# Kernel tuning notes

Measured on AMD Instinct MI355X. Metric: run time of the kernel, lower is better.

The kernel has to match this reference:

```python
import jax, jax.numpy as jnp
import numpy as np

N_QUBITS = 4
N_LAYERS = 2
KERNEL = 2
OUT_DEPTH = 4
SEED = 42          # pennylane RandomLayers default seed
RATIO_IMPRIM = 0.3 # pennylane RandomLayers default CNOT ratio


def _build_random_layers():
    """Replicates pennylane.templates.RandomLayers gate-structure sampling
    (seed=42): per layer, draw rotations from {RX,RY,RZ} on random wires
    (consuming one weight each) interleaved with CNOTs on random wire pairs."""
    rng = np.random.RandomState(SEED)
    rot_names = ['RX', 'RY', 'RZ']
    ops = []  # (name, wires, layer, weight_idx)
    for l in range(N_LAYERS):
        i = 0
        while i < 4:  # weights.shape[1] == 4
            if rng.random_sample() > RATIO_IMPRIM:
                gate = rot_names[rng.randint(3)]
                wire = int(rng.randint(N_QUBITS))
                ops.append((gate, (wire,), l, i))
                i += 1
            else:
                w = rng.choice(N_QUBITS, size=2, replace=False)
                ops.append(('CNOT', (int(w[0]), int(w[1])), l, -1))
    return tuple(ops)

OPS = _build_random_layers()

_CNOT = np.array([[1, 0, 0, 0], [0, 1, 0, 0], [0, 0, 0, 1], [0, 0, 1, 0]], dtype=np.complex64)


def _apply_1q(state, U, wire):
    # state: [P, 2,2,2,2]; U: [P,2,2] (batched) or [2,2] (shared)
    st = jnp.moveaxis(state, 1 + wire, -1)
    if U.ndim == 3:
        st = jnp.einsum('pab,p...b->p...a', U, st)
    else:
        st = jnp.einsum('ab,p...b->p...a', U, st)
    return jnp.moveaxis(st, -1, 1 + wire)


def _apply_cnot(state, c, t):
    st = jnp.moveaxis(state, (1 + c, 1 + t), (-2, -1))
    shp = st.shape
    st = st.reshape(shp[:-2] + (4,))
    st = jnp.einsum('ab,p...b->p...a', jnp.asarray(_CNOT), st)
    return jnp.moveaxis(st.reshape(shp), (-2, -1), (1 + c, 1 + t))


def _ry_batched(theta):
    # theta [P] -> [P,2,2]  (RY is real)
    c = jnp.cos(theta / 2)
    s = jnp.sin(theta / 2)
    return jnp.stack([jnp.stack([c, -s], -1), jnp.stack([s, c], -1)], -2).astype(jnp.complex64)


def _rot(name, theta):
    th = theta.astype(jnp.float32)
    c = jnp.cos(th / 2).astype(jnp.complex64)
    s = jnp.sin(th / 2).astype(jnp.complex64)
    zero = c * 0
    if name == 'RX':
        return jnp.stack([jnp.stack([c, -1j * s]), jnp.stack([-1j * s, c])])
    if name == 'RY':
        return jnp.stack([jnp.stack([c, -s]), jnp.stack([s, c])])
    # RZ
    e_m = jnp.exp(-0.5j * th.astype(jnp.complex64))
    e_p = jnp.exp(0.5j * th.astype(jnp.complex64))
    return jnp.stack([jnp.stack([e_m, zero]), jnp.stack([zero, e_p])])


def _patches(x):
    # x [1,C,H,W] -> [C*out*out, s*s], row-major pixel order matching
    # flatten(x[0, c, idx:idx+s, idy:idy+s])
    out = x.shape[3] - KERNEL + 1
    cols = [x[0, :, i:i + out, j:j + out] for i in range(KERNEL) for j in range(KERNEL)]
    p = jnp.stack(cols, axis=-1)  # [C, out, out, s*s]
    return p.reshape(-1, KERNEL * KERNEL)


def _simulate(angles, weights):
    # angles [P, n_qubits] -> PauliZ expectations [P, n_qubits]
    P = angles.shape[0]
    state = jnp.zeros((P,) + (2,) * N_QUBITS, jnp.complex64)
    state = state.at[(slice(None),) + (0,) * N_QUBITS].set(1.0)
    for j in range(N_QUBITS):  # angle encoding: RY(pi * input_j)
        state = _apply_1q(state, _ry_batched(angles[:, j]), j)
    for (name, wires, l, wi) in OPS:  # RandomLayers(weights)
        if name == 'CNOT':
            state = _apply_cnot(state, wires[0], wires[1])
        else:
            state = _apply_1q(state, _rot(name, weights[l, wi]), wires[0])
    probs = state.real ** 2 + state.imag ** 2  # [P,2,2,2,2]
    z = jnp.array([1.0, -1.0], probs.dtype)
    exps = []
    for j in range(N_QUBITS):
        other = tuple(a for a in range(1, 1 + N_QUBITS) if a != 1 + j)
        exps.append(probs.sum(axis=other) @ z)  # [P]
    return jnp.stack(exps, -1)  # [P, n_qubits]


def setup_inputs() -> dict:
    key = jax.random.key(0)
    kx, kw = jax.random.split(key)
    x = jax.random.uniform(kx, (1, 3, 512, 512), jnp.float32)
    weights = jax.random.uniform(kw, (N_LAYERS, 4), jnp.float32, 0.0, float(2 * np.pi))
    return {"x": x, "weights": weights}


def reference(x, weights):
    out_hw = x.shape[3] - KERNEL + 1
    C = x.shape[1]
    angles = jnp.pi * _patches(x)              # [C*out*out, 4]
    exps = _simulate(angles, weights)          # [C*out*out, 4]
    q_out = exps.reshape(C, out_hw, out_hw, KERNEL * KERNEL).sum(0)  # channel sum, as the idz loop
    # exact torch.reshape semantics: row-major reinterpretation of (out,out,4)
    return q_out.reshape(1, OUT_DEPTH, out_hw, out_hw)
```

## Files before the change

### kernel.cpp

```cpp
#include <hip/hip_runtime.h>
#include <stdint.h>

#define OUTHW 511
#define IMGW 512

struct COps { int n; int kind[64]; int wa[64]; int wb[64]; int widx[64]; };

struct CMT {
    uint32_t mt[624]; int mti;
    constexpr CMT(uint32_t s) : mt{}, mti(624) {
        mt[0] = s;
        for (int i = 1; i < 624; ++i)
            mt[i] = 1812433253u * (mt[i - 1] ^ (mt[i - 1] >> 30)) + (uint32_t)i;
    }
    constexpr uint32_t next32() {
        if (mti >= 624) {
            for (int i = 0; i < 624; ++i) {
                uint32_t y = (mt[i] & 0x80000000u) | (mt[(i + 1) % 624] & 0x7fffffffu);
                mt[i] = mt[(i + 397) % 624] ^ (y >> 1) ^ ((y & 1u) ? 0x9908b0dfu : 0u);
            }
            mti = 0;
        }
        uint32_t y = mt[mti++];
        y ^= y >> 11; y ^= (y << 7) & 0x9d2c5680u; y ^= (y << 15) & 0xefc60000u; y ^= y >> 18;
        return y;
    }
    constexpr double rand_double() {
        uint32_t a = next32() >> 5, b = next32() >> 6;
        return (a * 67108864.0 + b) / 9007199254740992.0;
    }
    constexpr uint32_t interval(uint32_t mx) {
        if (mx == 0) return 0;
        uint32_t mask = mx;
        mask |= mask >> 1; mask |= mask >> 2; mask |= mask >> 4;
        mask |= mask >> 8; mask |= mask >> 16;
        uint32_t v = next32() & mask;
        while (v > mx) v = next32() & mask;
        return v;
    }
};

constexpr COps build_ops_ce() {
    CMT mt(42u); COps P{}; P.n = 0;
    for (int l = 0; l < 2; ++l) {
        int i = 0;
        while (i < 4 && P.n < 64) {
            if (mt.rand_double() > 0.3) {
                int g = (int)mt.interval(2);
                int w = (int)mt.interval(3);
                P.kind[P.n] = g; P.wa[P.n] = w; P.wb[P.n] = 0; P.widx[P.n] = l * 4 + i;
                ++P.n; ++i;
            } else {
                int arr[4] = {0, 1, 2, 3};
                for (int ii = 3; ii >= 1; --ii) {
                    int j = (int)mt.interval((uint32_t)ii);
                    int t = arr[ii]; arr[ii] = arr[j]; arr[j] = t;
                }
                P.kind[P.n] = 3; P.wa[P.n] = arr[0]; P.wb[P.n] = arr[1]; P.widx[P.n] = -1;
                ++P.n;
            }
        }
    }
    return P;
}
constexpr COps OPS = build_ops_ce();

struct Tabs {
    bool u[81];
    bool mj[4][81];
    int nu;
    int tlist[81];
    int zm[81], xm[81];
};

constexpr Tabs build_tabs() {
    Tabs T{};
    for (int j = 0; j < 4; ++j) {
        bool cur[256] = {};
        cur[1 << (4 + j)] = true;
        for (int o = OPS.n - 1; o >= 0; --o) {
            bool nxt[256] = {};
            for (int c = 0; c < 256; ++c) if (cur[c]) {
                if (OPS.kind[o] == 3) {
                    int cc = OPS.wa[o], tt = OPS.wb[o], nc = c;
                    if (c & (1 << cc))       nc ^= (1 << tt);
                    if (c & (1 << (4 + tt))) nc ^= (1 << (4 + cc));
                    nxt[nc] = true;
                } else {
                    int w = OPS.wa[o];
                    int xw = (c >> w) & 1, zw = (c >> (4 + w)) & 1;
                    bool anti = false; int pm = 0;
                    if (OPS.kind[o] == 0)      { anti = zw != 0;        pm = 1 << w; }
                    else if (OPS.kind[o] == 1) { anti = (xw ^ zw) != 0; pm = (1 << w) | (1 << (4 + w)); }
                    else                       { anti = xw != 0;        pm = 1 << (4 + w); }
                    nxt[c] = true;
                    if (anti) nxt[c ^ pm] = true;
                }
            }
            for (int c = 0; c < 256; ++c) cur[c] = nxt[c];
        }
        for (int c = 0; c < 256; ++c) if (cur[c]) {
            bool hasY = false; int t = 0;
            for (int k = 0; k < 4; ++k) {
                int xk = (c >> k) & 1, zk = (c >> (4 + k)) & 1;
                if (xk && zk) hasY = true;
                t = t * 3 + (zk ? 1 : (xk ? 2 : 0));
            }
            if (!hasY) { T.mj[j][t] = true; T.u[t] = true; }
        }
    }
    T.nu = 0;
    for (int t = 0; t < 81; ++t) {
        int dd[4] = {t / 27, (t / 9) % 3, (t / 3) % 3, t % 3};
        int zm = 0, xm = 0;
        for (int k = 0; k < 4; ++k) {
            int p = 3 - k;
            if (dd[k] == 1) zm |= 1 << p;
            else if (dd[k] == 2) xm |= 1 << p;
        }
        T.zm[t] = zm; T.xm[t] = xm;
        if (T.u[t]) T.tlist[T.nu++] = t;
    }
    return T;
}
constexpr Tabs TB = build_tabs();
constexpr int NU = TB.nu;

__device__ float g_W[4 * 81];

__global__ void __launch_bounds__(512) build_table(const float* __restrict__ wts) {
    __shared__ float Ur[256];
    __shared__ float Ui[256];
    __shared__ float S[81 * 16];
    const int tid = threadIdx.x;
    if (tid < 256) {
        Ur[tid] = ((tid >> 4) == (tid & 15)) ? 1.f : 0.f;
        Ui[tid] = 0.f;
    }
    __syncthreads();
    const float INV4PI = 0.07957747154594767f;
#pragma unroll
    for (int o = 0; o < OPS.n; ++o) {
        if (OPS.kind[o] == 3) {
            const int pc = 3 - OPS.wa[o], pt = 3 - OPS.wb[o];
            if (tid < 64) {
                int b = tid >> 2, q = tid & 3;
                int rem[2]; int ri = 0;
#pragma unroll
                for (int p = 0; p < 4; ++p) if (p != pc && p != pt) rem[ri++] = p;
                int n  = (1 << pc) | ((q & 1) ? (1 << rem[0]) : 0)
                                   | (((q >> 1) & 1) ? (1 << rem[1]) : 0);
                int n2 = n | (1 << pt);
                float tr = Ur[b * 16 + n]; Ur[b * 16 + n] = Ur[b * 16 + n2]; Ur[b * 16 + n2] = tr;
                float ti = Ui[b * 16 + n]; Ui[b * 16 + n] = Ui[b * 16 + n2]; Ui[b * 16 + n2] = ti;
            }
        } else {
            const float th = wts[OPS.widx[o]];
            const float ch = __builtin_amdgcn_cosf(th * INV4PI);
            const float sh = __builtin_amdgcn_sinf(th * INV4PI);
            const int p = 3 - OPS.wa[o];
            if (tid < 128) {
                int b = tid >> 3, q = tid & 7;
                int low = q & ((1 << p) - 1);
                int high = (q >> p) << (p + 1);
                int n0 = high | low, n1 = n0 | (1 << p);
                float a0r = Ur[b * 16 + n0], a0i = Ui[b * 16 + n0];
                float a1r = Ur[b * 16 + n1], a1i = Ui[b * 16 + n1];
                float b0r, b0i, b1r, b1i;
                if (OPS.kind[o] == 0) {
                    b0r = ch * a0r + sh * a1i;  b0i = ch * a0i - sh * a1r;
                    b1r = sh * a0i + ch * a1r;  b1i = -sh * a0r + ch * a1i;
                } else if (OPS.kind[o] == 1) {
                    b0r = ch * a0r - sh * a1r;  b0i = ch * a0i - sh * a1i;
                    b1r = sh * a0r + ch * a1r;  b1i = sh * a0i + ch * a1i;
                } else {
                    b0r = ch * a0r + sh * a0i;  b0i = ch * a0i - sh * a0r;
                    b1r = ch * a1r - sh * a1i;  b1i = ch * a1i + sh * a1r;
                }
                Ur[b * 16 + n0] = b0r; Ui[b * 16 + n0] = b0i;
                Ur[b * 16 + n1] = b1r; Ui[b * 16 + n1] = b1i;
            }
        }
        __syncthreads();
    }
    for (int item = tid; item < NU * 16; item += 512) {
        const int t = TB.tlist[item >> 4], n = item & 15;
        const int zmask = TB.zm[t], xmask = TB.xm[t];
        float s = 0.f;
#pragma unroll
        for (int b2 = 0; b2 < 16; ++b2) {
            int bx = b2 ^ xmask;
            float sgn = (__popc(b2 & zmask) & 1) ? -1.f : 1.f;
            s += sgn * (Ur[b2 * 16 + n] * Ur[bx * 16 + n] +
                        Ui[b2 * 16 + n] * Ui[bx * 16 + n]);
        }
        S[t * 16 + n] = s;
    }
    __syncthreads();
    for (int item = tid; item < 324; item += 512) {
        const int j = item / 81, t = item % 81;
        if (!TB.mj[j][t]) continue;
        float acc = 0.f;
#pragma unroll
        for (int n = 0; n < 16; ++n) {
            float zj = ((n >> (3 - j)) & 1) ? -1.f : 1.f;
            acc += zj * S[t * 16 + n];
        }
        g_W[item] = acc * 0.0625f;
    }
}

__global__ void __launch_bounds__(256) quanv_kernel(const float* __restrict__ x,
                                                    float* __restrict__ out) {
    const int j = blockIdx.x * blockDim.x + threadIdx.x;
    const int i = blockIdx.y;
    if (j >= OUTHW) return;

    float mon[81];
#pragma unroll
    for (int t = 0; t < 81; ++t) mon[t] = 0.f;

#pragma unroll
    for (int c = 0; c < 3; ++c) {
        const float* xc = x + (size_t)c * (IMGW * IMGW);
        const float p00 = xc[i * IMGW + j];
        const float p01 = xc[i * IMGW + j + 1];
        const float p10 = xc[(i + 1) * IMGW + j];
        const float p11 = xc[(i + 1) * IMGW + j + 1];
        const float c0 = __builtin_amdgcn_cosf(0.5f * p00), s0 = __builtin_amdgcn_sinf(0.5f * p00);
        const float c1 = __builtin_amdgcn_cosf(0.5f * p01), s1 = __builtin_amdgcn_sinf(0.5f * p01);
        const float c2 = __builtin_amdgcn_cosf(0.5f * p10), s2 = __builtin_amdgcn_sinf(0.5f * p10);
        const float c3 = __builtin_amdgcn_cosf(0.5f * p11), s3 = __builtin_amdgcn_sinf(0.5f * p11);
        const float v0[3] = {1.f, c0, s0};
        const float v1[3] = {1.f, c1, s1};
        const float v2[3] = {1.f, c2, s2};
        const float v3[3] = {1.f, c3, s3};
        float m01[9], m23[9];
#pragma unroll
        for (int a = 0; a < 3; ++a)
#pragma unroll
            for (int b = 0; b < 3; ++b) {
                m01[a * 3 + b] = v0[a] * v1[b];
                m23[a * 3 + b] = v2[a] * v3[b];
            }
#pragma unroll
        for (int a = 0; a < 9; ++a)
#pragma unroll
            for (int b = 0; b < 9; ++b)
                if (TB.u[a * 9 + b])
                    mon[a * 9 + b] = fmaf(m01[a], m23[b], mon[a * 9 + b]);
    }

    float acc0 = 0.f, acc1 = 0.f, acc2 = 0.f, acc3 = 0.f;
#pragma unroll
    for (int t = 0; t < 81; ++t) {
        if (TB.mj[0][t]) acc0 = fmaf(g_W[0 * 81 + t], mon[t], acc0);
        if (TB.mj[1][t]) acc1 = fmaf(g_W[1 * 81 + t], mon[t], acc1);
        if (TB.mj[2][t]) acc2 = fmaf(g_W[2 * 81 + t], mon[t], acc2);
        if (TB.mj[3][t]) acc3 = fmaf(g_W[3 * 81 + t], mon[t], acc3);
    }
    float4 o = make_float4(acc0, acc1, acc2, acc3);
    *reinterpret_cast<float4*>(out + (size_t)(i * OUTHW + j) * 4) = o;
}

extern "C" void kernel_launch(void* const* d_in, const int* in_sizes, int n_in,
                              void* d_out, int out_size, void* d_ws, size_t ws_size,
                              hipStream_t stream) {
    const float* x   = (const float*)d_in[0];
    const float* wts = (const float*)d_in[1];
    float* out = (float*)d_out;

    hipLaunchKernelGGL(build_table, dim3(1), dim3(512), 0, stream, wts);

    dim3 grid((OUTHW + 255) / 256, OUTHW);
    hipLaunchKernelGGL(quanv_kernel, grid, dim3(256), 0, stream, x, out);
}
```

Measured before the change: 12.80 us.

## Share per-pixel sin/cos across threads via shared-memory tile

Each block now covers a 2x128 output tile. It first computes cos/sin of every input pixel in a 3x129 halo per channel once and stores them in shared memory. Each thread then reads its four neighbours from LDS instead of doing four global loads and eight transcendental evaluations per channel. This cuts redundant trig work and global loads by roughly 4x, at the cost of a __syncthreads, LDS traffic, and clamped halo loads at the image edges.

After: 13.47 us. 1.05x slower.

```diff
diff --git a/kernel.cpp b/kernel.cpp
--- a/kernel.cpp
+++ b/kernel.cpp
@@ -210,31 +210,55 @@
     }
 }
 
+#define TJ 128
+#define TI 2
 __global__ void __launch_bounds__(256) quanv_kernel(const float* __restrict__ x,
                                                     float* __restrict__ out) {
-    const int j = blockIdx.x * blockDim.x + threadIdx.x;
-    const int i = blockIdx.y;
-    if (j >= OUTHW) return;
+    __shared__ float2 trig[3][3][TJ + 4];
+    const int j0 = blockIdx.x * TJ;
+    const int i0 = blockIdx.y * TI;
+    const int tid = threadIdx.x;
+
+#pragma unroll
+    for (int ch = 0; ch < 3; ++ch) {
+        const float* xc = x + (size_t)ch * (IMGW * IMGW);
+#pragma unroll
+        for (int base = 0; base < 387; base += 256) {
+            int idx = base + tid;
+            if (idx < 387) {
+                int r = (idx >= 258) ? 2 : (idx >= 129 ? 1 : 0);
+                int c = idx - r * 129;
+                int gi = i0 + r; if (gi > 511) gi = 511;
+                int gj = j0 + c; if (gj > 511) gj = 511;
+                float v = 0.5f * xc[gi * IMGW + gj];
+                float2 t;
+                t.x = __builtin_amdgcn_cosf(v);
+                t.y = __builtin_amdgcn_sinf(v);
+                trig[ch][r][c] = t;
+            }
+        }
+    }
+    __syncthreads();
+
+    const int lj = tid & (TJ - 1);
+    const int li = tid >> 7;
+    const int j = j0 + lj;
+    const int i = i0 + li;
 
     float mon[81];
 #pragma unroll
     for (int t = 0; t < 81; ++t) mon[t] = 0.f;
 
 #pragma unroll
-    for (int c = 0; c < 3; ++c) {
-        const float* xc = x + (size_t)c * (IMGW * IMGW);
-        const float p00 = xc[i * IMGW + j];
-        const float p01 = xc[i * IMGW + j + 1];
-        const float p10 = xc[(i + 1) * IMGW + j];
-        const float p11 = xc[(i + 1) * IMGW + j + 1];
-        const float c0 = __builtin_amdgcn_cosf(0.5f * p00), s0 = __builtin_amdgcn_sinf(0.5f * p00);
-        const float c1 = __builtin_amdgcn_cosf(0.5f * p01), s1 = __builtin_amdgcn_sinf(0.5f * p01);
-        const float c2 = __builtin_amdgcn_cosf(0.5f * p10), s2 = __builtin_amdgcn_sinf(0.5f * p10);
-        const float c3 = __builtin_amdgcn_cosf(0.5f * p11), s3 = __builtin_amdgcn_sinf(0.5f * p11);
-        const float v0[3] = {1.f, c0, s0};
-        const float v1[3] = {1.f, c1, s1};
-        const float v2[3] = {1.f, c2, s2};
-        const float v3[3] = {1.f, c3, s3};
+    for (int ch = 0; ch < 3; ++ch) {
+        const float2 a00 = trig[ch][li][lj];
+        const float2 a01 = trig[ch][li][lj + 1];
+        const float2 a10 = trig[ch][li + 1][lj];
+        const float2 a11 = trig[ch][li + 1][lj + 1];
+        const float v0[3] = {1.f, a00.x, a00.y};
+        const float v1[3] = {1.f, a01.x, a01.y};
+        const float v2[3] = {1.f, a10.x, a10.y};
+        const float v3[3] = {1.f, a11.x, a11.y};
         float m01[9], m23[9];
 #pragma unroll
         for (int a = 0; a < 3; ++a)
@@ -259,8 +283,10 @@
         if (TB.mj[2][t]) acc2 = fmaf(g_W[2 * 81 + t], mon[t], acc2);
         if (TB.mj[3][t]) acc3 = fmaf(g_W[3 * 81 + t], mon[t], acc3);
     }
-    float4 o = make_float4(acc0, acc1, acc2, acc3);
-    *reinterpret_cast<float4*>(out + (size_t)(i * OUTHW + j) * 4) = o;
+    if (i < OUTHW && j < OUTHW) {
+        float4 o = make_float4(acc0, acc1, acc2, acc3);
+        *reinterpret_cast<float4*>(out + (size_t)(i * OUTHW + j) * 4) = o;
+    }
 }
 
 extern "C" void kernel_launch(void* const* d_in, const int* in_sizes, int n_in,
@@ -272,6 +298,6 @@
 
     hipLaunchKernelGGL(build_table, dim3(1), dim3(512), 0, stream, wts);
 
-    dim3 grid((OUTHW + 255) / 256, OUTHW);
+    dim3 grid((OUTHW + TJ - 1) / TJ, (OUTHW + TI - 1) / TI);
     hipLaunchKernelGGL(quanv_kernel, grid, dim3(256), 0, stream, x, out);
 }
```

## Fuse weight-table construction into main kernel, recomputing per block in LDS

Applied to the files above, without the earlier changes.

Removes the separate single-block build_table launch by having every block of the main kernel rebuild the 4x81 observable weight table in shared memory. Each block first computes its per-pixel monomials, then simulates the circuit unitary and the Pauli-sum table cooperatively, and finally reads the weights as float4 from LDS. This saves a kernel launch and the dependency between the two kernels. In exchange every one of ~1000 blocks repeats the unitary simulation and several barriers, and uses more LDS.

Measured after the change: 12.02 us. 1.06x faster.

```diff
diff --git a/kernel.cpp b/kernel.cpp
--- a/kernel.cpp
+++ b/kernel.cpp
@@ -126,17 +126,56 @@
 constexpr Tabs TB = build_tabs();
 constexpr int NU = TB.nu;
 
-__device__ float g_W[4 * 81];
-
-__global__ void __launch_bounds__(512) build_table(const float* __restrict__ wts) {
+__global__ void __launch_bounds__(256) quanv_fused(const float* __restrict__ x,
+                                                   const float* __restrict__ wts,
+                                                   float* __restrict__ out) {
     __shared__ float Ur[256];
     __shared__ float Ui[256];
     __shared__ float S[81 * 16];
+    __shared__ __align__(16) float Wl[81][4];
+
     const int tid = threadIdx.x;
-    if (tid < 256) {
-        Ur[tid] = ((tid >> 4) == (tid & 15)) ? 1.f : 0.f;
-        Ui[tid] = 0.f;
-    }
+    const int j = blockIdx.x * blockDim.x + tid;
+    const int i = blockIdx.y;
+    const int jj = (j < OUTHW) ? j : (OUTHW - 1);
+
+    float mon[81];
+#pragma unroll
+    for (int t = 0; t < 81; ++t) mon[t] = 0.f;
+
+#pragma unroll
+    for (int c = 0; c < 3; ++c) {
+        const float* xc = x + (size_t)c * (IMGW * IMGW);
+        const float p00 = xc[i * IMGW + jj];
+        const float p01 = xc[i * IMGW + jj + 1];
+        const float p10 = xc[(i + 1) * IMGW + jj];
+        const float p11 = xc[(i + 1) * IMGW + jj + 1];
+        const float c0 = __builtin_amdgcn_cosf(0.5f * p00), s0 = __builtin_amdgcn_sinf(0.5f * p00);
+        const float c1 = __builtin_amdgcn_cosf(0.5f * p01), s1 = __builtin_amdgcn_sinf(0.5f * p01);
+        const float c2 = __builtin_amdgcn_cosf(0.5f * p10), s2 = __builtin_amdgcn_sinf(0.5f * p10);
+        const float c3 = __builtin_amdgcn_cosf(0.5f * p11), s3 = __builtin_amdgcn_sinf(0.5f * p11);
+        const float v0[3] = {1.f, c0, s0};
+        const float v1[3] = {1.f, c1, s1};
+        const float v2[3] = {1.f, c2, s2};
+        const float v3[3] = {1.f, c3, s3};
+        float m01[9], m23[9];
+#pragma unroll
+        for (int a = 0; a < 3; ++a)
+#pragma unroll
+            for (int b = 0; b < 3; ++b) {
+                m01[a * 3 + b] = v0[a] * v1[b];
+                m23[a * 3 + b] = v2[a] * v3[b];
+            }
+#pragma unroll
+        for (int a = 0; a < 9; ++a)
+#pragma unroll
+            for (int b = 0; b < 9; ++b)
+                if (TB.u[a * 9 + b])
+                    mon[a * 9 + b] = fmaf(m01[a], m23[b], mon[a * 9 + b]);
+    }
+
+    Ur[tid] = ((tid >> 4) == (tid & 15)) ? 1.f : 0.f;
+    Ui[tid] = 0.f;
     __syncthreads();
     const float INV4PI = 0.07957747154594767f;
 #pragma unroll
@@ -183,7 +222,7 @@
         }
         __syncthreads();
     }
-    for (int item = tid; item < NU * 16; item += 512) {
+    for (int item = tid; item < NU * 16; item += 256) {
         const int t = TB.tlist[item >> 4], n = item & 15;
         const int zmask = TB.zm[t], xmask = TB.xm[t];
         float s = 0.f;
@@ -197,67 +236,32 @@
         S[t * 16 + n] = s;
     }
     __syncthreads();
-    for (int item = tid; item < 324; item += 512) {
-        const int j = item / 81, t = item % 81;
-        if (!TB.mj[j][t]) continue;
+    for (int item = tid; item < 324; item += 256) {
+        const int jo = item / 81, t = item % 81;
         float acc = 0.f;
-#pragma unroll
-        for (int n = 0; n < 16; ++n) {
-            float zj = ((n >> (3 - j)) & 1) ? -1.f : 1.f;
-            acc += zj * S[t * 16 + n];
-        }
-        g_W[item] = acc * 0.0625f;
-    }
-}
-
-__global__ void __launch_bounds__(256) quanv_kernel(const float* __restrict__ x,
-                                                    float* __restrict__ out) {
-    const int j = blockIdx.x * blockDim.x + threadIdx.x;
-    const int i = blockIdx.y;
+        if (TB.mj[jo][t]) {
+#pragma unroll
+            for (int n = 0; n < 16; ++n) {
+                float zj = ((n >> (3 - jo)) & 1) ? -1.f : 1.f;
+                acc += zj * S[t * 16 + n];
+            }
+            acc *= 0.0625f;
+        }
+        Wl[t][jo] = acc;
+    }
+    __syncthreads();
+
     if (j >= OUTHW) return;
-
-    float mon[81];
-#pragma unroll
-    for (int t = 0; t < 81; ++t) mon[t] = 0.f;
-
-#pragma unroll
-    for (int c = 0; c < 3; ++c) {
-        const float* xc = x + (size_t)c * (IMGW * IMGW);
-        const float p00 = xc[i * IMGW + j];
-        const float p01 = xc[i * IMGW + j + 1];
-        const float p10 = xc[(i + 1) * IMGW + j];
-        const float p11 = xc[(i + 1) * IMGW + j + 1];
-        const float c0 = __builtin_amdgcn_cosf(0.5f * p00), s0 = __builtin_amdgcn_sinf(0.5f * p00);
-        const float c1 = __builtin_amdgcn_cosf(0.5f * p01), s1 = __builtin_amdgcn_sinf(0.5f * p01);
-        const float c2 = __builtin_amdgcn_cosf(0.5f * p10), s2 = __builtin_amdgcn_sinf(0.5f * p10);
-        const float c3 = __builtin_amdgcn_cosf(0.5f * p11), s3 = __builtin_amdgcn_sinf(0.5f * p11);
-        const float v0[3] = {1.f, c0, s0};
-        const float v1[3] = {1.f, c1, s1};
-        const float v2[3] = {1.f, c2, s2};
-        const float v3[3] = {1.f, c3, s3};
-        float m01[9], m23[9];
-#pragma unroll
-        for (int a = 0; a < 3; ++a)
-#pragma unroll
-            for (int b = 0; b < 3; ++b) {
-                m01[a * 3 + b] = v0[a] * v1[b];
-                m23[a * 3 + b] = v2[a] * v3[b];
-            }
-#pragma unroll
-        for (int a = 0; a < 9; ++a)
-#pragma unroll
-            for (int b = 0; b < 9; ++b)
-                if (TB.u[a * 9 + b])
-                    mon[a * 9 + b] = fmaf(m01[a], m23[b], mon[a * 9 + b]);
-    }
-
     float acc0 = 0.f, acc1 = 0.f, acc2 = 0.f, acc3 = 0.f;
 #pragma unroll
     for (int t = 0; t < 81; ++t) {
-        if (TB.mj[0][t]) acc0 = fmaf(g_W[0 * 81 + t], mon[t], acc0);
-        if (TB.mj[1][t]) acc1 = fmaf(g_W[1 * 81 + t], mon[t], acc1);
-        if (TB.mj[2][t]) acc2 = fmaf(g_W[2 * 81 + t], mon[t], acc2);
-        if (TB.mj[3][t]) acc3 = fmaf(g_W[3 * 81 + t], mon[t], acc3);
+        if (!TB.u[t]) continue;
+        const float4 w = *reinterpret_cast<const float4*>(&Wl[t][0]);
+        const float m = mon[t];
+        if (TB.mj[0][t]) acc0 = fmaf(w.x, m, acc0);
+        if (TB.mj[1][t]) acc1 = fmaf(w.y, m, acc1);
+        if (TB.mj[2][t]) acc2 = fmaf(w.z, m, acc2);
+        if (TB.mj[3][t]) acc3 = fmaf(w.w, m, acc3);
     }
     float4 o = make_float4(acc0, acc1, acc2, acc3);
     *reinterpret_cast<float4*>(out + (size_t)(i * OUTHW + j) * 4) = o;
@@ -270,8 +274,6 @@
     const float* wts = (const float*)d_in[1];
     float* out = (float*)d_out;
 
-    hipLaunchKernelGGL(build_table, dim3(1), dim3(512), 0, stream, wts);
-
     dim3 grid((OUTHW + 255) / 256, OUTHW);
-    hipLaunchKernelGGL(quanv_kernel, grid, dim3(256), 0, stream, x, out);
-}
+    hipLaunchKernelGGL(quanv_fused, grid, dim3(256), 0, stream, x, wts, out);
+}
```
